# Kernel tuning notes

Measured on AMD Instinct MI355X. Metric: run time of the kernel, lower is better.

Reference implementation:

```python
import jax, jax.numpy as jnp
import numpy as np

T, A, B, N = 16, 64, 64, 12
BATCH, ZS, ENC, DEC = 4096, 100, 400, 400


def setup_inputs() -> dict:
    key = jax.random.key(0)
    ks = jax.random.split(key, 20)
    s = 0.05  # small init so exp(log_sigma)/exp(log_delta) stay well-behaved
    rn = lambda k, shp: s * jax.random.normal(k, shp, dtype=jnp.float32)
    return {
        "x": jax.random.uniform(ks[0], (BATCH, A * B), dtype=jnp.float32),
        "eps": jax.random.normal(ks[1], (T, BATCH, ZS), dtype=jnp.float32),
        # encoder LSTMCell: input = read(2*N*N) concat h_dec(DEC)
        "w_enc_ih": rn(ks[2], (4 * ENC, 2 * N * N + DEC)),
        "w_enc_hh": rn(ks[3], (4 * ENC, ENC)),
        "b_enc_ih": jnp.zeros((4 * ENC,), jnp.float32),
        "b_enc_hh": jnp.zeros((4 * ENC,), jnp.float32),
        # decoder LSTMCell: input = z(ZS)
        "w_dec_ih": rn(ks[4], (4 * DEC, ZS)),
        "w_dec_hh": rn(ks[5], (4 * DEC, DEC)),
        "b_dec_ih": jnp.zeros((4 * DEC,), jnp.float32),
        "b_dec_hh": jnp.zeros((4 * DEC,), jnp.float32),
        "w_mu": rn(ks[6], (ZS, ENC)),
        "b_mu": jnp.zeros((ZS,), jnp.float32),
        "w_sig": rn(ks[7], (ZS, ENC)),
        "b_sig": jnp.zeros((ZS,), jnp.float32),
        "w_attn": rn(ks[8], (5, DEC)),
        "b_attn": jnp.zeros((5,), jnp.float32),
        "w_write": rn(ks[9], (N * N, DEC)),
        "b_write": jnp.zeros((N * N,), jnp.float32),
    }


def _lstm(inp, h, c, wi, wh, bi, bh):
    # PyTorch LSTMCell gate order: i, f, g, o
    g = inp @ wi.T + bi + h @ wh.T + bh
    i, f, gg, o = jnp.split(g, 4, axis=-1)
    c2 = jax.nn.sigmoid(f) * c + jax.nn.sigmoid(i) * jnp.tanh(gg)
    h2 = jax.nn.sigmoid(o) * jnp.tanh(c2)
    return h2, c2


def reference(x, eps, w_enc_ih, w_enc_hh, b_enc_ih, b_enc_hh,
              w_dec_ih, w_dec_hh, b_dec_ih, b_dec_hh,
              w_mu, b_mu, w_sig, b_sig, w_attn, b_attn, w_write, b_write):
    batch = x.shape[0]
    rng = jnp.arange(N, dtype=x.dtype)        # (N,)
    grid_a = jnp.arange(A, dtype=x.dtype)     # (A,)
    grid_b = jnp.arange(B, dtype=x.dtype)     # (B,)
    half = N / 2 + 0.5

    def attn(h_dec):
        p = h_dec @ w_attn.T + b_attn                       # (b,5)
        gx_, gy_, ls2, ld, lg = [p[:, i:i + 1] for i in range(5)]
        gx = (A + 1) / 2 * (gx_ + 1)
        gy = (B + 1) / 2 * (gy_ + 1)
        delta = (max(A, B) - 1) / (N - 1) * jnp.exp(ld)     # (b,1)
        sigma2 = jnp.exp(ls2)[:, :, None]                   # (b,1,1)
        gamma = jnp.exp(lg)                                  # (b,1)
        mu_x = (rng[None, :] - half) * delta + gx            # (b,N)
        mu_y = (rng[None, :] - half) * delta + gy

        def fb(grid, mu):
            t = (grid[None, None, :] - mu[:, :, None]) / (2 * sigma2)
            F = jnp.exp(-t * t)                              # (b,N,len)
            return F / (F.sum(2, keepdims=True) + 1e-9)
        return fb(grid_a, mu_x), fb(grid_b, mu_y), gamma

    def step(carry, eps_t):
        c, h_enc, s_enc, h_dec, s_dec = carry
        x_hat = x - jax.nn.sigmoid(c)
        Fx, Fy, gamma = attn(h_dec)

        def glimpse(img):  # Fy @ img @ Fx^T, scaled by gamma
            g = jnp.einsum('bnB,bBA,bmA->bnm', Fy, img.reshape(-1, B, A), Fx)
            return g.reshape(-1, N * N) * gamma

        r = jnp.concatenate([glimpse(x), glimpse(x_hat)], axis=1)  # (b,2*N*N)
        h_enc, s_enc = _lstm(jnp.concatenate([r, h_dec], axis=1),
                             h_enc, s_enc, w_enc_ih, w_enc_hh, b_enc_ih, b_enc_hh)
        mu = h_enc @ w_mu.T + b_mu
        logsig = h_enc @ w_sig.T + b_sig
        z = mu + jnp.exp(logsig) * eps_t
        h_dec, s_dec = _lstm(z, h_dec, s_dec, w_dec_ih, w_dec_hh, b_dec_ih, b_dec_hh)
        Fx2, Fy2, gamma2 = attn(h_dec)
        w = (h_dec @ w_write.T + b_write).reshape(-1, N, N)
        wr = jnp.einsum('bnB,bnm,bmA->bBA', Fy2, w, Fx2).reshape(-1, A * B) / gamma2
        return (c + wr, h_enc, s_enc, h_dec, s_dec), None

    zf = lambda d: jnp.zeros((batch, d), x.dtype)
    init = (jnp.zeros_like(x), zf(ENC), zf(ENC), zf(DEC), zf(DEC))
    (c, _, _, _, _), _ = jax.lax.scan(step, init, eps)
    return c  # final canvas logits, shape (batch, A*B)
```

## Files before the change

### kernel.cpp

```cpp
#include <hip/hip_runtime.h>
#include <cstdint>
#include <cstddef>

#define T_STEPS 16
#define AA 64
#define BBX 64
#define NF 12
#define BATCH 4096
#define ZS 100
#define ENC 400
#define DEC 400
#define IMG (AA*BBX)
#define RDIM (2*NF*NF)
#define GDIM (4*ENC)

#define KENC 1088
#define KDEC 544
#define KSML 416
#define NBIG 1664
#define NSML 256

typedef __attribute__((ext_vector_type(8))) short bfrag;
typedef __attribute__((ext_vector_type(4))) float f32x4;

__device__ __forceinline__ float sigmoidf_(float v) { return 1.f / (1.f + expf(-v)); }

__device__ __forceinline__ float bf2f(unsigned short u) {
    uint32_t x = ((uint32_t)u) << 16;
    return __builtin_bit_cast(float, x);
}

__device__ __forceinline__ void split2(float f, unsigned short& h, unsigned short& l) {
    uint32_t u = __builtin_bit_cast(uint32_t, f);
    uint32_t hb = (u + 0x7FFFu + ((u >> 16) & 1u)) >> 16;
    float hf = __builtin_bit_cast(float, hb << 16);
    float r = f - hf;
    uint32_t v = __builtin_bit_cast(uint32_t, r);
    uint32_t lb = (v + 0x7FFFu + ((v >> 16) & 1u)) >> 16;
    h = (unsigned short)hb;
    l = (unsigned short)lb;
}

__global__ __launch_bounds__(256, 2) void k_gemm2(
    const unsigned short* __restrict__ Ah, const unsigned short* __restrict__ Al,
    int lda, int a_off,
    const unsigned short* __restrict__ Bh, const unsigned short* __restrict__ Bl,
    int Kpad,
    const float* __restrict__ b1, const float* __restrict__ b2,
    float* __restrict__ C, int NN)
{
    __shared__ unsigned short lA[2][8 * 512];
    __shared__ unsigned short lB[2][8 * 512];

    const int tid = threadIdx.x;
    const int lane = tid & 63;
    const int wave = tid >> 6;
    const int wr = wave >> 1;
    const int wc = wave & 1;
    const int m0 = blockIdx.y * 128;
    const int n0 = blockIdx.x * 128;
    const int rlow = lane & 15;
    const int kg8 = (lane >> 4) * 8;

    const size_t aBase = (size_t)(m0 + rlow) * lda + a_off + kg8;
    const size_t bBase = (size_t)(n0 + rlow) * Kpad + kg8;
    const unsigned short* gsrc;
    unsigned short* ldst;
    size_t stride16;
    if (wave == 0)      { gsrc = Ah + aBase; ldst = &lA[0][0]; stride16 = (size_t)lda * 16; }
    else if (wave == 1) { gsrc = Al + aBase; ldst = &lA[1][0]; stride16 = (size_t)lda * 16; }
    else if (wave == 2) { gsrc = Bh + bBase; ldst = &lB[0][0]; stride16 = (size_t)Kpad * 16; }
    else                { gsrc = Bl + bBase; ldst = &lB[1][0]; stride16 = (size_t)Kpad * 16; }

    f32x4 acc[4][4];
#pragma unroll
    for (int mf = 0; mf < 4; ++mf)
#pragma unroll
        for (int nf = 0; nf < 4; ++nf) acc[mf][nf] = (f32x4){0.f, 0.f, 0.f, 0.f};

    for (int k0 = 0; k0 < Kpad; k0 += 32) {
#pragma unroll
        for (int sub = 0; sub < 8; ++sub) {
            __builtin_amdgcn_global_load_lds(
                (const __attribute__((address_space(1))) void*)(gsrc + (size_t)sub * stride16 + k0),
                (__attribute__((address_space(3))) void*)(ldst + sub * 512), 16, 0, 0);
        }
        __syncthreads();

        bfrag bhf[4], blf[4];
#pragma unroll
        for (int nf = 0; nf < 4; ++nf) {
            bhf[nf] = *(const bfrag*)&lB[0][(wc * 4 + nf) * 512 + lane * 8];
            blf[nf] = *(const bfrag*)&lB[1][(wc * 4 + nf) * 512 + lane * 8];
        }
#pragma unroll
        for (int mf = 0; mf < 4; ++mf) {
            const bfrag ah = *(const bfrag*)&lA[0][(wr * 4 + mf) * 512 + lane * 8];
            const bfrag al = *(const bfrag*)&lA[1][(wr * 4 + mf) * 512 + lane * 8];
#pragma unroll
            for (int nf = 0; nf < 4; ++nf) {
                acc[mf][nf] = __builtin_amdgcn_mfma_f32_16x16x32_bf16(ah, bhf[nf], acc[mf][nf], 0, 0, 0);
                acc[mf][nf] = __builtin_amdgcn_mfma_f32_16x16x32_bf16(ah, blf[nf], acc[mf][nf], 0, 0, 0);
                acc[mf][nf] = __builtin_amdgcn_mfma_f32_16x16x32_bf16(al, bhf[nf], acc[mf][nf], 0, 0, 0);
            }
        }
        __syncthreads();
    }

    const int col = lane & 15;
    const int rowq = (lane >> 4) * 4;
#pragma unroll
    for (int nf = 0; nf < 4; ++nf) {
        const int n = n0 + wc * 64 + nf * 16 + col;
        if (n < NN) {
            float bb = b1[n];
            if (b2) bb += b2[n];
#pragma unroll
            for (int mf = 0; mf < 4; ++mf) {
                const int mbase = m0 + wr * 64 + mf * 16 + rowq;
#pragma unroll
                for (int j = 0; j < 4; ++j)
                    C[(size_t)(mbase + j) * NN + n] = acc[mf][nf][j] + bb;
            }
        }
    }
}

__global__ __launch_bounds__(256) void k_fillw(
    const float* __restrict__ src, int rows, int cols,
    unsigned short* __restrict__ dh, unsigned short* __restrict__ dl,
    int ld, int col0, int row0)
{
    const int i = blockIdx.x * 256 + threadIdx.x;
    if (i >= rows * cols) return;
    const int r = i / cols, c = i - r * cols;
    unsigned short h, l;
    split2(src[i], h, l);
    dh[(size_t)(row0 + r) * ld + col0 + c] = h;
    dl[(size_t)(row0 + r) * ld + col0 + c] = l;
}

__device__ __forceinline__ void attn_compute(
    const float* __restrict__ hd,
    const float* __restrict__ w_attn, const float* __restrict__ b_attn,
    float* __restrict__ p,
    float (* __restrict__ Fx)[68], float (* __restrict__ Fy)[68],
    float* __restrict__ rowinv)
{
    const int t = threadIdx.x;
    const int lane = t & 63, wave = t >> 6;
    for (int o = wave; o < 5; o += 4) {
        float s = 0.f;
        for (int k = lane; k < DEC; k += 64) s += hd[k] * w_attn[o * DEC + k];
#pragma unroll
        for (int off = 32; off; off >>= 1) s += __shfl_down(s, off);
        if (lane == 0) p[o] = s + b_attn[o];
    }
    __syncthreads();
    const float gx = 32.5f * (p[0] + 1.f);
    const float gy = 32.5f * (p[1] + 1.f);
    const float sigma2 = expf(p[2]);
    const float delta = (63.f / 11.f) * expf(p[3]);
    const float inv2s = 1.f / (2.f * sigma2);
    for (int e = t; e < NF * 64; e += 256) {
        const int n = e >> 6, a = e & 63;
        const float mu_x = ((float)n - 6.5f) * delta + gx;
        const float mu_y = ((float)n - 6.5f) * delta + gy;
        const float tx = ((float)a - mu_x) * inv2s;
        const float ty = ((float)a - mu_y) * inv2s;
        Fx[n][a] = expf(-tx * tx);
        Fy[n][a] = expf(-ty * ty);
    }
    __syncthreads();
    for (int rix = wave; rix < 24; rix += 4) {
        const float* row = (rix < 12) ? &Fx[rix][0] : &Fy[rix - 12][0];
        float s = row[lane];
#pragma unroll
        for (int off = 32; off; off >>= 1) s += __shfl_down(s, off);
        if (lane == 0) rowinv[rix] = 1.f / (s + 1e-9f);
    }
    __syncthreads();
    for (int e = t; e < NF * 64; e += 256) {
        const int n = e >> 6, a = e & 63;
        Fx[n][a] *= rowinv[n];
        Fy[n][a] *= rowinv[12 + n];
    }
}

__global__ __launch_bounds__(256) void k_glimpse(
    const float* __restrict__ x, const float* __restrict__ c,
    unsigned short* __restrict__ eAh, unsigned short* __restrict__ eAl,
    const float* __restrict__ w_attn, const float* __restrict__ b_attn)
{
    __shared__ __align__(16) float hd[DEC];
    __shared__ __align__(16) float p[8];
    __shared__ __align__(16) float Fx[NF][68], Fy[NF][68];
    __shared__ __align__(16) float rowinv[24];
    __shared__ __align__(16) float img[IMG], imgh[IMG];
    __shared__ __align__(16) float tmp1[NF][68], tmp2[NF][68];
    const int item = blockIdx.x;
    const int t = threadIdx.x;
    const size_t arow = (size_t)item * KENC;

    for (int i = t; i < DEC; i += 256)
        hd[i] = bf2f(eAh[arow + 288 + i]) + bf2f(eAl[arow + 288 + i]);
    __syncthreads();
    attn_compute(hd, w_attn, b_attn, p, Fx, Fy, rowinv);

    for (int i = t; i < IMG; i += 256) {
        const float xv = x[(size_t)item * IMG + i];
        const float cv = c[(size_t)item * IMG + i];
        img[i] = xv;
        imgh[i] = xv - sigmoidf_(cv);
    }
    __syncthreads();
    const float gamma = expf(p[4]);

    if (t < 192) {
        const int n = t >> 4, a0 = (t & 15) * 4;
        float s10 = 0, s11 = 0, s12 = 0, s13 = 0;
        float s20 = 0, s21 = 0, s22 = 0, s23 = 0;
        for (int Bi = 0; Bi < 64; ++Bi) {
            const float fy = Fy[n][Bi];
            const float4 v1 = *(const float4*)&img[Bi * 64 + a0];
            const float4 v2 = *(const float4*)&imgh[Bi * 64 + a0];
            s10 += fy * v1.x; s11 += fy * v1.y; s12 += fy * v1.z; s13 += fy * v1.w;
            s20 += fy * v2.x; s21 += fy * v2.y; s22 += fy * v2.z; s23 += fy * v2.w;
        }
        *(float4*)&tmp1[n][a0] = make_float4(s10, s11, s12, s13);
        *(float4*)&tmp2[n][a0] = make_float4(s20, s21, s22, s23);
    }
    __syncthreads();

    for (int e = t; e < 2 * NF * NF; e += 256) {
        const int which = e / 144;
        const int idx = e - which * 144;
        const int n = idx / 12, m = idx - (idx / 12) * 12;
        const float (*tp)[68] = which ? tmp2 : tmp1;
        const float4* tv = (const float4*)&tp[n][0];
        const float4* fv = (const float4*)&Fx[m][0];
        float s = 0.f;
#pragma unroll
        for (int a4 = 0; a4 < 16; ++a4) {
            const float4 tvv = tv[a4], fvv = fv[a4];
            s += tvv.x * fvv.x + tvv.y * fvv.y + tvv.z * fvv.z + tvv.w * fvv.w;
        }
        unsigned short vh, vl;
        split2(s * gamma, vh, vl);
        eAh[arow + e] = vh;
        eAl[arow + e] = vl;
    }
}

__global__ __launch_bounds__(256) void k_lstm(
    const float* __restrict__ gates, float* __restrict__ s,
    unsigned short* __restrict__ d1h, unsigned short* __restrict__ d1l, int ld1,
    unsigned short* __restrict__ d2h, unsigned short* __restrict__ d2l, int ld2)
{
    const int idx = blockIdx.x * 256 + threadIdx.x;
    if (idx >= BATCH * ENC) return;
    const int m = idx / ENC, n = idx - m * ENC;
    const float* g = gates + (size_t)m * GDIM;
    const float gi = g[n], gf = g[n + 400], gg = g[n + 800], go = g[n + 1200];
    const float cold = s[idx];
    const float c2 = sigmoidf_(gf) * cold + sigmoidf_(gi) * tanhf(gg);
    s[idx] = c2;
    const float h = sigmoidf_(go) * tanhf(c2);
    unsigned short hh, hl;
    split2(h, hh, hl);
    d1h[(size_t)m * ld1 + n] = hh;
    d1l[(size_t)m * ld1 + n] = hl;
    if (d2h) {
        d2h[(size_t)m * ld2 + n] = hh;
        d2l[(size_t)m * ld2 + n] = hl;
    }
}

__global__ __launch_bounds__(256) void k_zelem(
    const float* __restrict__ mus, const float* __restrict__ eps_t,
    unsigned short* __restrict__ dzh, unsigned short* __restrict__ dzl)
{
    const int idx = blockIdx.x * 256 + threadIdx.x;
    if (idx >= BATCH * ZS) return;
    const int m = idx / ZS, o = idx - m * ZS;
    const float zv = mus[(size_t)m * 200 + o] + expf(mus[(size_t)m * 200 + 100 + o]) * eps_t[idx];
    unsigned short h, l;
    split2(zv, h, l);
    dzh[(size_t)m * KDEC + o] = h;
    dzl[(size_t)m * KDEC + o] = l;
}

__global__ __launch_bounds__(256) void k_write(
    const unsigned short* __restrict__ eAh, const unsigned short* __restrict__ eAl,
    const float* __restrict__ w_attn, const float* __restrict__ b_attn,
    const float* __restrict__ wvec,
    float* __restrict__ c)
{
    __shared__ __align__(16) float hd[DEC];
    __shared__ __align__(16) float p[8];
    __shared__ __align__(16) float Fx[NF][68], Fy[NF][68];
    __shared__ __align__(16) float rowinv[24];
    __shared__ __align__(16) float wsv[NF * NF];
    __shared__ __align__(16) float u[64][13];
    const int item = blockIdx.x;
    const int t = threadIdx.x;
    const size_t arow = (size_t)item * KENC;

    for (int i = t; i < DEC; i += 256)
        hd[i] = bf2f(eAh[arow + 288 + i]) + bf2f(eAl[arow + 288 + i]);
    if (t < NF * NF) wsv[t] = wvec[(size_t)item * (NF * NF) + t];
    __syncthreads();
    attn_compute(hd, w_attn, b_attn, p, Fx, Fy, rowinv);
    __syncthreads();
    const float ginv = 1.f / expf(p[4]);

    for (int e = t; e < 64 * NF; e += 256) {
        const int Bb = e / 12, m = e - (e / 12) * 12;
        float s = 0.f;
#pragma unroll
        for (int n = 0; n < 12; ++n) s += Fy[n][Bb] * wsv[n * 12 + m];
        u[Bb][m] = s;
    }
    __syncthreads();
    for (int i = t; i < IMG; i += 256) {
        const int Bb = i >> 6, a = i & 63;
        float s = 0.f;
#pragma unroll
        for (int m = 0; m < 12; ++m) s += u[Bb][m] * Fx[m][a];
        c[(size_t)item * IMG + i] += s * ginv;
    }
}

extern "C" void kernel_launch(void* const* d_in, const int* in_sizes, int n_in,
                              void* d_out, int out_size, void* d_ws, size_t ws_size,
                              hipStream_t stream)
{
    const float* x        = (const float*)d_in[0];
    const float* eps      = (const float*)d_in[1];
    const float* w_enc_ih = (const float*)d_in[2];
    const float* w_enc_hh = (const float*)d_in[3];
    const float* b_enc_ih = (const float*)d_in[4];
    const float* b_enc_hh = (const float*)d_in[5];
    const float* w_dec_ih = (const float*)d_in[6];
    const float* w_dec_hh = (const float*)d_in[7];
    const float* b_dec_ih = (const float*)d_in[8];
    const float* b_dec_hh = (const float*)d_in[9];
    const float* w_mu     = (const float*)d_in[10];
    const float* b_mu     = (const float*)d_in[11];
    const float* w_sig    = (const float*)d_in[12];
    const float* b_sig    = (const float*)d_in[13];
    const float* w_attn   = (const float*)d_in[14];
    const float* b_attn   = (const float*)d_in[15];
    const float* w_write  = (const float*)d_in[16];
    const float* b_write  = (const float*)d_in[17];

    float* canvas = (float*)d_out;

    uint8_t* p = (uint8_t*)d_ws;
    auto nextu = [&](size_t elems) {
        unsigned short* r = (unsigned short*)p;
        p += (elems * 2 + 255) & ~(size_t)255;
        return r;
    };
    auto nextf = [&](size_t elems) {
        float* r = (float*)p;
        p += (elems * 4 + 255) & ~(size_t)255;
        return r;
    };
    uint8_t* zstart = p;
    unsigned short* encA_h = nextu((size_t)(BATCH + 1) * KENC);
    unsigned short* encA_l = nextu((size_t)(BATCH + 1) * KENC);
    unsigned short* decA_h = nextu((size_t)(BATCH + 1) * KDEC);
    unsigned short* decA_l = nextu((size_t)(BATCH + 1) * KDEC);
    unsigned short* encB_h = nextu((size_t)NBIG * KENC);
    unsigned short* encB_l = nextu((size_t)NBIG * KENC);
    unsigned short* decB_h = nextu((size_t)NBIG * KDEC);
    unsigned short* decB_l = nextu((size_t)NBIG * KDEC);
    unsigned short* musB_h = nextu((size_t)NSML * KSML);
    unsigned short* musB_l = nextu((size_t)NSML * KSML);
    unsigned short* wrtB_h = nextu((size_t)NSML * KSML);
    unsigned short* wrtB_l = nextu((size_t)NSML * KSML);
    float* s_enc = nextf((size_t)BATCH * ENC);
    float* s_dec = nextf((size_t)BATCH * DEC);
    float* b_cat = nextf(256);
    uint8_t* zend = p;
    float* gates = nextf((size_t)BATCH * GDIM);
    float* mus   = nextf((size_t)BATCH * 200);
    float* wvec  = nextf((size_t)BATCH * (NF * NF));

    hipMemsetAsync(zstart, 0, (size_t)(zend - zstart), stream);
    hipMemsetAsync(canvas, 0, (size_t)BATCH * IMG * sizeof(float), stream);

    auto fill = [&](const float* src, int rows, int cols,
                    unsigned short* dh, unsigned short* dl, int ld, int col0, int row0) {
        k_fillw<<<dim3((rows * cols + 255) / 256), 256, 0, stream>>>(
            src, rows, cols, dh, dl, ld, col0, row0);
    };
    fill(w_enc_ih, 1600, 688, encB_h, encB_l, KENC, 0, 0);
    fill(w_enc_hh, 1600, 400, encB_h, encB_l, KENC, 688, 0);
    fill(w_dec_ih, 1600, 100, decB_h, decB_l, KDEC, 0, 0);
    fill(w_dec_hh, 1600, 400, decB_h, decB_l, KDEC, 128, 0);
    fill(w_mu,     100, 400, musB_h, musB_l, KSML, 0, 0);
    fill(w_sig,    100, 400, musB_h, musB_l, KSML, 0, 100);
    fill(w_write,  144, 400, wrtB_h, wrtB_l, KSML, 0, 0);
    hipMemcpyAsync(b_cat,       b_mu,  100 * 4, hipMemcpyDeviceToDevice, stream);
    hipMemcpyAsync(b_cat + 100, b_sig, 100 * 4, hipMemcpyDeviceToDevice, stream);

    const dim3 blk(256);
    for (int t = 0; t < T_STEPS; ++t) {
        k_glimpse<<<BATCH, blk, 0, stream>>>(x, canvas, encA_h, encA_l, w_attn, b_attn);
        k_gemm2<<<dim3(13, 32), blk, 0, stream>>>(encA_h, encA_l, KENC, 0,
            encB_h, encB_l, KENC, b_enc_ih, b_enc_hh, gates, GDIM);
        k_lstm<<<dim3((BATCH * ENC + 255) / 256), blk, 0, stream>>>(gates, s_enc,
            encA_h + 688, encA_l + 688, KENC, nullptr, nullptr, 0);
        k_gemm2<<<dim3(2, 32), blk, 0, stream>>>(encA_h, encA_l, KENC, 688,
            musB_h, musB_l, KSML, b_cat, nullptr, mus, 200);
        k_zelem<<<dim3((BATCH * ZS + 255) / 256), blk, 0, stream>>>(
            mus, eps + (size_t)t * BATCH * ZS, decA_h, decA_l);
        k_gemm2<<<dim3(13, 32), blk, 0, stream>>>(decA_h, decA_l, KDEC, 0,
            decB_h, decB_l, KDEC, b_dec_ih, b_dec_hh, gates, GDIM);
        k_lstm<<<dim3((BATCH * ENC + 255) / 256), blk, 0, stream>>>(gates, s_dec,
            encA_h + 288, encA_l + 288, KENC, decA_h + 128, decA_l + 128, KDEC);
        k_gemm2<<<dim3(2, 32), blk, 0, stream>>>(encA_h, encA_l, KENC, 288,
            wrtB_h, wrtB_l, KSML, b_write, nullptr, wvec, NF * NF);
        k_write<<<BATCH, blk, 0, stream>>>(encA_h, encA_l, w_attn, b_attn, wvec, canvas);
    }
}
```

Before: 4.692 ms.

## Fuse canvas write with next step's glimpse read in one kernel

Adds a k_wrgl kernel that applies the write update to the canvas and then immediately computes the next timestep's glimpse from the same in-LDS canvas and image. The attention filters are computed once and shared, since the write and the next read both use the same h_dec. The fused kernel also loads x and c into LDS with direct global-to-LDS loads. This removes one kernel launch, one canvas re-read and one attention recomputation per step. The cost is a larger LDS footprint of about 40KB per block, which may lower occupancy.

```diff
diff --git a/kernel.cpp b/kernel.cpp
--- a/kernel.cpp
+++ b/kernel.cpp
@@ -39,6 +39,12 @@
     uint32_t lb = (v + 0x7FFFu + ((v >> 16) & 1u)) >> 16;
     h = (unsigned short)hb;
     l = (unsigned short)lb;
+}
+
+__device__ __forceinline__ void bar_lds() {
+    asm volatile("s_waitcnt lgkmcnt(0)" ::: "memory");
+    __builtin_amdgcn_s_barrier();
+    __builtin_amdgcn_sched_barrier(0);
 }
 
 __global__ __launch_bounds__(256, 2) void k_gemm2(
@@ -187,6 +193,53 @@
     }
 }
 
+__device__ __forceinline__ void attn_compute_nb(
+    const float* __restrict__ hd,
+    const float* __restrict__ w_attn, const float* __restrict__ b_attn,
+    float* __restrict__ p,
+    float (* __restrict__ Fx)[68], float (* __restrict__ Fy)[68],
+    float* __restrict__ rowinv)
+{
+    const int t = threadIdx.x;
+    const int lane = t & 63, wave = t >> 6;
+    for (int o = wave; o < 5; o += 4) {
+        float s = 0.f;
+        for (int k = lane; k < DEC; k += 64) s += hd[k] * w_attn[o * DEC + k];
+#pragma unroll
+        for (int off = 32; off; off >>= 1) s += __shfl_down(s, off);
+        if (lane == 0) p[o] = s + b_attn[o];
+    }
+    bar_lds();
+    const float gx = 32.5f * (p[0] + 1.f);
+    const float gy = 32.5f * (p[1] + 1.f);
+    const float sigma2 = expf(p[2]);
+    const float delta = (63.f / 11.f) * expf(p[3]);
+    const float inv2s = 1.f / (2.f * sigma2);
+    for (int e = t; e < NF * 64; e += 256) {
+        const int n = e >> 6, a = e & 63;
+        const float mu_x = ((float)n - 6.5f) * delta + gx;
+        const float mu_y = ((float)n - 6.5f) * delta + gy;
+        const float tx = ((float)a - mu_x) * inv2s;
+        const float ty = ((float)a - mu_y) * inv2s;
+        Fx[n][a] = expf(-tx * tx);
+        Fy[n][a] = expf(-ty * ty);
+    }
+    bar_lds();
+    for (int rix = wave; rix < 24; rix += 4) {
+        const float* row = (rix < 12) ? &Fx[rix][0] : &Fy[rix - 12][0];
+        float s = row[lane];
+#pragma unroll
+        for (int off = 32; off; off >>= 1) s += __shfl_down(s, off);
+        if (lane == 0) rowinv[rix] = 1.f / (s + 1e-9f);
+    }
+    bar_lds();
+    for (int e = t; e < NF * 64; e += 256) {
+        const int n = e >> 6, a = e & 63;
+        Fx[n][a] *= rowinv[n];
+        Fy[n][a] *= rowinv[12 + n];
+    }
+}
+
 __global__ __launch_bounds__(256) void k_glimpse(
     const float* __restrict__ x, const float* __restrict__ c,
     unsigned short* __restrict__ eAh, unsigned short* __restrict__ eAl,
@@ -232,6 +285,122 @@
     }
     __syncthreads();
 
+    for (int e = t; e < 2 * NF * NF; e += 256) {
+        const int which = e / 144;
+        const int idx = e - which * 144;
+        const int n = idx / 12, m = idx - (idx / 12) * 12;
+        const float (*tp)[68] = which ? tmp2 : tmp1;
+        const float4* tv = (const float4*)&tp[n][0];
+        const float4* fv = (const float4*)&Fx[m][0];
+        float s = 0.f;
+#pragma unroll
+        for (int a4 = 0; a4 < 16; ++a4) {
+            const float4 tvv = tv[a4], fvv = fv[a4];
+            s += tvv.x * fvv.x + tvv.y * fvv.y + tvv.z * fvv.z + tvv.w * fvv.w;
+        }
+        unsigned short vh, vl;
+        split2(s * gamma, vh, vl);
+        eAh[arow + e] = vh;
+        eAl[arow + e] = vl;
+    }
+}
+
+__global__ __launch_bounds__(256) void k_wrgl(
+    const float* __restrict__ x, float* __restrict__ c,
+    unsigned short* __restrict__ eAh, unsigned short* __restrict__ eAl,
+    const float* __restrict__ w_attn, const float* __restrict__ b_attn,
+    const float* __restrict__ wvec)
+{
+    __shared__ __align__(16) float xx[IMG];
+    __shared__ __align__(16) float cc[IMG];
+    __shared__ __align__(16) float hd[DEC];
+    __shared__ __align__(16) float p[8];
+    __shared__ __align__(16) float Fx[NF][68], Fy[NF][68];
+    __shared__ __align__(16) float rowinv[24];
+    __shared__ __align__(16) float wsv[NF * NF];
+    __shared__ __align__(16) float u[64][13];
+    __shared__ __align__(16) float tmp1[NF][68], tmp2[NF][68];
+    const int item = blockIdx.x;
+    const int t = threadIdx.x;
+    const int lane = t & 63, wave = t >> 6;
+    const size_t arow = (size_t)item * KENC;
+
+    float hdv0 = 0.f, hdv1 = 0.f, wv0 = 0.f;
+    {
+        const int i0 = t, i1 = t + 256;
+        hdv0 = bf2f(eAh[arow + 288 + i0]) + bf2f(eAl[arow + 288 + i0]);
+        if (i1 < DEC) hdv1 = bf2f(eAh[arow + 288 + i1]) + bf2f(eAl[arow + 288 + i1]);
+        if (t < NF * NF) wv0 = wvec[(size_t)item * (NF * NF) + t];
+    }
+    {
+        const float* csrc = c + (size_t)item * IMG + wave * 1024 + lane * 4;
+        const float* xsrc = x + (size_t)item * IMG + wave * 1024 + lane * 4;
+        float* cdst = cc + wave * 1024;
+        float* xdst = xx + wave * 1024;
+#pragma unroll
+        for (int j = 0; j < 4; ++j) {
+            __builtin_amdgcn_global_load_lds(
+                (const __attribute__((address_space(1))) void*)(csrc + j * 256),
+                (__attribute__((address_space(3))) void*)(cdst + j * 256), 16, 0, 0);
+            __builtin_amdgcn_global_load_lds(
+                (const __attribute__((address_space(1))) void*)(xsrc + j * 256),
+                (__attribute__((address_space(3))) void*)(xdst + j * 256), 16, 0, 0);
+        }
+    }
+    hd[t] = hdv0;
+    if (t + 256 < DEC) hd[t + 256] = hdv1;
+    if (t < NF * NF) wsv[t] = wv0;
+    bar_lds();
+
+    attn_compute_nb(hd, w_attn, b_attn, p, Fx, Fy, rowinv);
+    bar_lds();
+    const float gamma = expf(p[4]);
+    const float ginv = 1.f / gamma;
+    for (int e = t; e < 64 * NF; e += 256) {
+        const int Bb = e / 12, m = e - (e / 12) * 12;
+        float s = 0.f;
+#pragma unroll
+        for (int n = 0; n < 12; ++n) s += Fy[n][Bb] * wsv[n * 12 + m];
+        u[Bb][m] = s;
+    }
+
+    __syncthreads();
+#pragma unroll
+    for (int j = 0; j < 4; ++j) {
+        const int i0 = j * 1024 + t * 4;
+        const int Bb = i0 >> 6, a0 = i0 & 63;
+        float s0 = 0, s1 = 0, s2 = 0, s3 = 0;
+#pragma unroll
+        for (int m = 0; m < 12; ++m) {
+            const float um = u[Bb][m];
+            s0 += um * Fx[m][a0];     s1 += um * Fx[m][a0 + 1];
+            s2 += um * Fx[m][a0 + 2]; s3 += um * Fx[m][a0 + 3];
+        }
+        const float4 cv = *(const float4*)&cc[i0];
+        const float4 cn = make_float4(cv.x + s0 * ginv, cv.y + s1 * ginv,
+                                      cv.z + s2 * ginv, cv.w + s3 * ginv);
+        *(float4*)&c[(size_t)item * IMG + i0] = cn;
+        const float4 xv = *(const float4*)&xx[i0];
+        *(float4*)&cc[i0] = make_float4(xv.x - sigmoidf_(cn.x), xv.y - sigmoidf_(cn.y),
+                                        xv.z - sigmoidf_(cn.z), xv.w - sigmoidf_(cn.w));
+    }
+    bar_lds();
+
+    if (t < 192) {
+        const int n = t >> 4, a0 = (t & 15) * 4;
+        float s10 = 0, s11 = 0, s12 = 0, s13 = 0;
+        float s20 = 0, s21 = 0, s22 = 0, s23 = 0;
+        for (int Bi = 0; Bi < 64; ++Bi) {
+            const float fy = Fy[n][Bi];
+            const float4 v1 = *(const float4*)&xx[Bi * 64 + a0];
+            const float4 v2 = *(const float4*)&cc[Bi * 64 + a0];
+            s10 += fy * v1.x; s11 += fy * v1.y; s12 += fy * v1.z; s13 += fy * v1.w;
+            s20 += fy * v2.x; s21 += fy * v2.y; s22 += fy * v2.z; s23 += fy * v2.w;
+        }
+        *(float4*)&tmp1[n][a0] = make_float4(s10, s11, s12, s13);
+        *(float4*)&tmp2[n][a0] = make_float4(s20, s21, s22, s23);
+    }
+    bar_lds();
     for (int e = t; e < 2 * NF * NF; e += 256) {
         const int which = e / 144;
         const int idx = e - which * 144;
@@ -407,8 +576,8 @@
     hipMemcpyAsync(b_cat + 100, b_sig, 100 * 4, hipMemcpyDeviceToDevice, stream);
 
     const dim3 blk(256);
+    k_glimpse<<<BATCH, blk, 0, stream>>>(x, canvas, encA_h, encA_l, w_attn, b_attn);
     for (int t = 0; t < T_STEPS; ++t) {
-        k_glimpse<<<BATCH, blk, 0, stream>>>(x, canvas, encA_h, encA_l, w_attn, b_attn);
         k_gemm2<<<dim3(13, 32), blk, 0, stream>>>(encA_h, encA_l, KENC, 0,
             encB_h, encB_l, KENC, b_enc_ih, b_enc_hh, gates, GDIM);
         k_lstm<<<dim3((BATCH * ENC + 255) / 256), blk, 0, stream>>>(gates, s_enc,
@@ -423,6 +592,12 @@
             encA_h + 288, encA_l + 288, KENC, decA_h + 128, decA_l + 128, KDEC);
         k_gemm2<<<dim3(2, 32), blk, 0, stream>>>(encA_h, encA_l, KENC, 288,
             wrtB_h, wrtB_l, KSML, b_write, nullptr, wvec, NF * NF);
-        k_write<<<BATCH, blk, 0, stream>>>(encA_h, encA_l, w_attn, b_attn, wvec, canvas);
-    }
-}
+        if (t < T_STEPS - 1) {
+            k_wrgl<<<BATCH, blk, 0, stream>>>(x, canvas, encA_h, encA_l,
+                                              w_attn, b_attn, wvec);
+        } else {
+            k_write<<<BATCH, blk, 0, stream>>>(encA_h, encA_l, w_attn, b_attn,
+                                               wvec, canvas);
+        }
+    }
+}
```

Measured after the change: 4.334 ms. 1.08x faster.
